# Optimization experiments

Measured on AMD Instinct MI355X. Metric: run time of the kernel, lower is better.

The kernel has to match this reference:

```python
import jax, jax.numpy as jnp
import numpy as np

HEAD_DIM = 16

def setup_inputs() -> dict:
    key = jax.random.key(0)
    ks = jax.random.split(key, 9)
    dim = 256
    B, H, W = 8, 32, 32
    x  = jax.random.normal(ks[0], (B, H, W, dim), jnp.float32)
    # Conv2d weights in OIHW layout (torch convention), small init
    w3 = jax.random.normal(ks[1], (dim, dim, 1, 1), jnp.float32) * 0.05
    b3 = jax.random.normal(ks[2], (dim,), jnp.float32) * 0.01
    w5 = jax.random.normal(ks[3], (dim, dim, 3, 3), jnp.float32) * 0.02
    b5 = jax.random.normal(ks[4], (dim,), jnp.float32) * 0.01
    w7 = jax.random.normal(ks[5], (dim, dim, 5, 5), jnp.float32) * 0.01
    b7 = jax.random.normal(ks[6], (dim,), jnp.float32) * 0.01
    # nn.Linear weight: (out_features=dim, in_features=attention_dim=dim), no bias
    wp = jax.random.normal(ks[7], (dim, dim), jnp.float32) * 0.05
    return {"x": x, "w3": w3, "b3": b3, "w5": w5, "b5": b5, "w7": w7, "b7": b7, "wp": wp}

def _conv2d_same(x_nchw, w_oihw, b):
    y = jax.lax.conv_general_dilated(
        x_nchw, w_oihw, window_strides=(1, 1), padding='SAME',
        dimension_numbers=('NCHW', 'OIHW', 'NCHW'))
    return y + b[None, :, None, None]

def reference(x, w3, b3, w5, b5, w7, b7, wp):
    B, H, W, C = x.shape
    N = H * W
    nh = C // HEAD_DIM            # num_heads
    scale = HEAD_DIM ** (-0.5)
    xc = jnp.transpose(x, (0, 3, 1, 2))  # NCHW
    # q: 1x1 conv, v: 3x3 conv, k: 5x5 conv (names match the torch code)
    q = _conv2d_same(xc, w3, b3).reshape(B, nh, N, HEAD_DIM)
    v = _conv2d_same(xc, w5, b5).reshape(B, nh, N, HEAD_DIM)
    k = _conv2d_same(xc, w7, b7).reshape(B, nh, N, HEAD_DIM)
    attn = jax.nn.softmax(jnp.einsum('bhnd,bhmd->bhnm', q, k) * scale, axis=-1)
    out = jnp.einsum('bhnm,bhmd->bhnd', attn, v)        # [B, nh, N, hd]
    out = jnp.transpose(out, (0, 2, 1, 3)).reshape(B, H, W, nh * HEAD_DIM)
    return out @ wp.T                                   # Linear, no bias
```

## Files before the change

kernel.cpp:

```cpp
#include <hip/hip_runtime.h>
#include <hip/hip_bf16.h>

#define DIM 256
#define HW  1024

typedef __attribute__((ext_vector_type(8))) short short8;
typedef __attribute__((ext_vector_type(4))) float floatx4;
typedef __attribute__((ext_vector_type(16))) float floatx16;
typedef __attribute__((address_space(1))) const unsigned int g_u32;
typedef __attribute__((address_space(3))) unsigned int l_u32;

#define QSCALE 0.36067376022224085f

__device__ inline unsigned short f2bf(float f) {
  union { float f; unsigned u; } v;
  v.f = f;
  unsigned u = v.u;
  u += 0x7fffu + ((u >> 16) & 1u);
  return (unsigned short)(u >> 16);
}

__device__ inline unsigned short f2bf_trunc(float f) {
  union { float f; unsigned u; } v;
  v.f = f;
  return (unsigned short)(v.u >> 16);
}

__device__ inline float ldin(const void* p, long i, int isf32) {
  if (isf32) return ((const float*)p)[i];
  union { unsigned u; float f; } v;
  v.u = ((unsigned)((const unsigned short*)p)[i]) << 16;
  return v.f;
}

__device__ inline int detect_inline(const unsigned short* __restrict__ xr,
                                    int* cnt) {
  if (threadIdx.x == 0) *cnt = 0;
  __syncthreads();
  int local = 0;
  for (int i = threadIdx.x; i < 8192; i += 256) {
    unsigned short u = xr[i];
    if ((u & 0x7F80u) == 0x7F80u) local++;
  }
  if (local) atomicAdd(cnt, local);
  __syncthreads();
  return (*cnt > 0) ? 1 : 0;
}

__device__ inline void frag_repack4(const void* __restrict__ w,
                                    unsigned short* __restrict__ wF, int KK,
                                    int slice, float* __restrict__ Wl,
                                    int isf32) {
  const int t = threadIdx.x;
  const int co16 = slice & 15;
  const int c8   = slice >> 4;
  const int RE = 32 * KK;
  const int RS = RE + 1;
  for (int g = 0; g < 4; ++g) {
    __syncthreads();
    for (int rloc = 0; rloc < 4; ++rloc) {
      const long base =
          ((long)((co16 * 16 + (g << 2) + rloc) * 256 + c8 * 32)) * KK;
      for (int i = t; i < RE; i += 256)
        Wl[rloc * RS + i] = ldin(w, base + i, isf32);
    }
    __syncthreads();
    for (int tap = 0; tap < KK; ++tap) {
      unsigned short* dst = wF + ((((tap << 3) + c8) << 4) + co16) * 512;
      if (t < 128) {
        const int colg = t >> 5;
        const int cis  = t & 31;
        const int col  = (g << 2) + colg;
        const int lane = ((cis >> 3) << 4) | col;
        const int j    = cis & 7;
        dst[lane * 8 + j] = f2bf(Wl[colg * RS + cis * KK + tap]);
      }
    }
  }
}

__global__ __launch_bounds__(256) void prep_kernel(
    const void* __restrict__ x,  const void* __restrict__ w3,
    const void* __restrict__ b3, const void* __restrict__ w5,
    const void* __restrict__ b5, const void* __restrict__ w7,
    const void* __restrict__ b7, const void* __restrict__ wp,
    unsigned short* __restrict__ xbf,
    unsigned short* __restrict__ wF3, unsigned short* __restrict__ wF5,
    unsigned short* __restrict__ wF7, unsigned short* __restrict__ wpF,
    float* __restrict__ bc, int* __restrict__ flag) {
  __shared__ float Wl[4 * 801];
  __shared__ int cnt;
  const int isf32 = detect_inline((const unsigned short*)x, &cnt);
  const int bid = blockIdx.x;
  const int t = threadIdx.x;
  if (bid < 512) {
#pragma unroll
    for (int r = 0; r < 4; ++r) {
      const int i = (bid * 1024 + r * 256 + t) * 4;
      if (isf32) {
        const float4 v = *(const float4*)((const float*)x + i);
        ushort4 o;
        o.x = f2bf(v.x); o.y = f2bf(v.y); o.z = f2bf(v.z); o.w = f2bf(v.w);
        *(ushort4*)(xbf + i) = o;
      } else {
        *(ushort4*)(xbf + i) =
            *(const ushort4*)((const unsigned short*)x + i);
      }
    }
  } else if (bid < 640) {
    frag_repack4(w7, wF7, 25, bid - 512, Wl, isf32);
  } else if (bid < 768) {
    frag_repack4(w5, wF5, 9, bid - 640, Wl, isf32);
  } else if (bid < 896) {
    frag_repack4(w3, wF3, 1, bid - 768, Wl, isf32);
  } else if (bid < 1024) {
    frag_repack4(wp, wpF, 1, bid - 896, Wl, isf32);
  } else {
#pragma unroll
    for (int r = 0; r < 3; ++r) {
      const int i = r * 256 + t;
      const void* src = (i < 256) ? b3 : (i < 512) ? b5 : b7;
      bc[i] = ldin(src, i & 255, isf32);
    }
    if (t == 0) *flag = isf32;
  }
}

__global__ __launch_bounds__(256, 2) void convqkv_kernel(
    const unsigned short* __restrict__ xbf,
    const unsigned short* __restrict__ wFq,
    const unsigned short* __restrict__ wFv,
    const unsigned short* __restrict__ wFk,
    const float* __restrict__ bc,
    unsigned short* __restrict__ qOut,
    unsigned short* __restrict__ vOut,
    unsigned short* __restrict__ kOut) {
  constexpr int WC = 36;
  constexpr int CELLS = 12 * WC;
  constexpr int LOADS = CELLS * 4;
  __shared__ unsigned short Xs[CELLS * 40];
  __shared__ unsigned short Bs[36 * 512];
  const int t    = threadIdx.x;
  const int bid  = blockIdx.x;
  const int cog0 = bid & 15;
  const int co0  = cog0 << 4;
  const int m0   = (bid >> 4) << 8;
  const int b    = m0 >> 10;
  const int n0   = m0 & 1023;
  const int r0   = n0 >> 5;
  const int wv   = t >> 6;
  const int lane = t & 63;
  const int l15  = lane & 15;
  const int quad = lane >> 4;

  floatx4 aq[4] = {}, av[4] = {}, ak[4] = {};

  for (int c8 = 0; c8 < 8; ++c8) {
    uint4 xreg[7];
#pragma unroll
    for (int rr = 0; rr < 7; ++rr) {
      const int id = rr * 256 + t;
      const int cell = id >> 2, part = id & 3;
      const int hr = cell / WC, wc = cell - hr * WC;
      const int xr = r0 + hr - 2, xc = wc - 2;
      const bool ok = (id < LOADS) && ((unsigned)xr < 32u) &&
                      ((unsigned)xc < 32u);
      const int cr = xr < 0 ? 0 : (xr > 31 ? 31 : xr);
      const int cc = xc < 0 ? 0 : (xc > 31 ? 31 : xc);
      uint4 v = *(const uint4*)&xbf[(((b * 32 + cr) * 32 + cc) << 8) +
                                    (c8 << 5) + (part << 3)];
      if (!ok) v = make_uint4(0, 0, 0, 0);
      xreg[rr] = v;
    }
    __syncthreads();
#pragma unroll
    for (int rr = 0; rr < 9; ++rr) {
      const int tap = (rr << 2) + wv;
      if (tap < 35) {
        const unsigned short* src;
        if (tap < 25) {
          src = &wFk[((((tap << 3) + c8) << 4) + cog0) * 512];
        } else if (tap < 34) {
          src = &wFv[(((((tap - 25) << 3) + c8) << 4) + cog0) * 512];
        } else {
          src = &wFq[((c8 << 4) + cog0) * 512];
        }
        __builtin_amdgcn_global_load_lds((g_u32*)(src + (lane << 3)),
                                         (l_u32*)&Bs[tap << 9], 16, 0, 0);
      }
    }
#pragma unroll
    for (int rr = 0; rr < 7; ++rr) {
      const int id = rr * 256 + t;
      if (id < LOADS)
        *(uint4*)&Xs[(id >> 2) * 40 + ((id & 3) << 3)] = xreg[rr];
    }
    __syncthreads();

#pragma unroll
    for (int tap = 0; tap < 25; ++tap) {
      const int kh = tap / 5, kw = tap % 5;
      const bool vv = (kh >= 1 && kh <= 3 && kw >= 1 && kw <= 3);
      short8 a[4];
#pragma unroll
      for (int rr2 = 0; rr2 < 2; ++rr2) {
#pragma unroll
        for (int ch = 0; ch < 2; ++ch) {
          const unsigned short* xs =
              &Xs[(((wv << 1) + rr2 + kh) * WC + (ch << 4) + l15 + kw) * 40 +
                  (quad << 3)];
          a[(rr2 << 1) + ch] = *(const short8*)xs;
        }
      }
      const short8 kb = *(const short8*)&Bs[(tap << 9) + (lane << 3)];
#pragma unroll
      for (int f = 0; f < 4; ++f)
        ak[f] = __builtin_amdgcn_mfma_f32_16x16x32_bf16(a[f], kb, ak[f],
                                                        0, 0, 0);
      if (vv) {
        const int vt = (kh - 1) * 3 + (kw - 1);
        const short8 vb = *(const short8*)&Bs[((25 + vt) << 9) + (lane << 3)];
#pragma unroll
        for (int f = 0; f < 4; ++f)
          av[f] = __builtin_amdgcn_mfma_f32_16x16x32_bf16(a[f], vb, av[f],
                                                          0, 0, 0);
      }
      if (tap == 12) {
        const short8 qb = *(const short8*)&Bs[(34 << 9) + (lane << 3)];
#pragma unroll
        for (int f = 0; f < 4; ++f)
          aq[f] = __builtin_amdgcn_mfma_f32_16x16x32_bf16(a[f], qb, aq[f],
                                                          0, 0, 0);
      }
    }
  }
#pragma unroll
  for (int rr2 = 0; rr2 < 2; ++rr2) {
#pragma unroll
    for (int ch = 0; ch < 2; ++ch) {
      const int f = (rr2 << 1) + ch;
      const int co = co0 + l15;
      const int slab = (b << 4) + (co >> 4);
      const int clo = co & 15;
      const int nb = n0 + (wv << 6) + (rr2 << 5) + (ch << 4) + (quad << 2);
      {
        const float bj = bc[co];
        floatx4 a = aq[f];
        ushort4 pk4;
        pk4.x = f2bf((a[0] + bj) * QSCALE);
        pk4.y = f2bf((a[1] + bj) * QSCALE);
        pk4.z = f2bf((a[2] + bj) * QSCALE);
        pk4.w = f2bf((a[3] + bj) * QSCALE);
        *(ushort4*)&qOut[(slab << 14) + (clo << 10) + nb] = pk4;
      }
      {
        const float bj = bc[512 + co];
        floatx4 a = ak[f];
        ushort4 pk4;
        pk4.x = f2bf(a[0] + bj); pk4.y = f2bf(a[1] + bj);
        pk4.z = f2bf(a[2] + bj); pk4.w = f2bf(a[3] + bj);
        *(ushort4*)&kOut[(slab << 14) + (clo << 10) + nb] = pk4;
      }
      {
        const float bj = bc[256 + co];
        floatx4 a = av[f];
        const int base = (slab << 14) + (clo << 6);
#pragma unroll
        for (int i = 0; i < 4; ++i) {
          const int n = nb + i;
          vOut[base + ((n & 15) << 10) + (n >> 4)] = f2bf(a[i] + bj);
        }
      }
    }
  }
}

__global__ __launch_bounds__(256, 4) void attn_mfma_kernel(
    const unsigned short* __restrict__ qg,
    const unsigned short* __restrict__ kg,
    const unsigned short* __restrict__ vg,
    unsigned short* __restrict__ out2) {
  __shared__ __align__(16) unsigned short Pb[4][32][40];
  const int t    = threadIdx.x;
  const int w    = t >> 6;
  const int lane = t & 63;
  const int slab = blockIdx.x >> 3;
  const int rb   = blockIdx.x & 7;
  const int b = slab >> 4;
  const int h = slab & 15;
  const int l31  = lane & 31;
  const int hl   = lane >> 5;
  const int l15  = lane & 15;
  const int quad = lane >> 4;

  const unsigned short* Kb = kg + (slab << 14);
  const unsigned short* Vb = vg + (slab << 14);

  const int row0 = (rb << 7) + (w << 5);
  const short8 qa =
      *(const short8*)&qg[(slab << 14) + ((row0 + l31) << 4) + (hl << 3)];

  const short onebf = (short)0x3F80;
  const short8 ones = {onebf, onebf, onebf, onebf, onebf, onebf, onebf, onebf};

  floatx4 acco[2] = {}, asum[2] = {};

  for (int kc = 0; kc < 1024; kc += 32) {
    const short8 kb = *(const short8*)&Kb[((kc + l31) << 4) + (hl << 3)];
    floatx16 s = {};
    s = __builtin_amdgcn_mfma_f32_32x32x16_bf16(qa, kb, s, 0, 0, 0);
#pragma unroll
    for (int r = 0; r < 16; ++r) {
      const float e = __builtin_amdgcn_exp2f(s[r]);
      const int row = (r & 3) + ((r >> 2) << 3) + (hl << 2);
      Pb[w][row][l31] = f2bf_trunc(e);
    }
    const short8 vb = *(const short8*)&Vb[(l15 << 10) + kc + (quad << 3)];
#pragma unroll
    for (int tt = 0; tt < 2; ++tt) {
      const short8 pa = *(const short8*)&Pb[w][(tt << 4) + l15][quad << 3];
      acco[tt] =
          __builtin_amdgcn_mfma_f32_16x16x32_bf16(pa, vb, acco[tt], 0, 0, 0);
      asum[tt] =
          __builtin_amdgcn_mfma_f32_16x16x32_bf16(pa, ones, asum[tt], 0, 0, 0);
    }
  }
#pragma unroll
  for (int tt = 0; tt < 2; ++tt) {
#pragma unroll
    for (int r = 0; r < 4; ++r) {
      const int nloc = (tt << 4) + (quad << 2) + r;
      const float val = acco[tt][r] / asum[tt][r];
      const int n = row0 + nloc;
      out2[(((b << 10) + n) << 8) + (h << 4) + l15] = f2bf(val);
    }
  }
}

__global__ __launch_bounds__(256) void linear_mfma_kernel(
    const unsigned short* __restrict__ inp,
    const unsigned short* __restrict__ wpF,
    void* __restrict__ out, const int* __restrict__ flag) {
  __shared__ unsigned short As[64 * 40];
  const int isf32 = *flag;
  const int t   = threadIdx.x;
  const int m0  = blockIdx.x << 6;
  const int co0 = blockIdx.y << 6;
  const int wv   = t >> 6;
  const int lane = t & 63;
  const int wm = (wv & 1) << 5;
  const int wn = (wv >> 1) << 5;
  const int l15  = lane & 15;
  const int quad = lane >> 4;
  const int cogb = (co0 >> 4) + (wn >> 4);
  const int rowS = t >> 2;
  const int partS = t & 3;

  floatx4 acc[2][2] = {};

  short8 cb0, cb1;
  {
    const unsigned short* wptr = &wpF[(cogb << 9) + (lane << 3)];
    cb0 = *(const short8*)wptr;
    cb1 = *(const short8*)(wptr + 512);
  }
  for (int c8 = 0; c8 < 8; ++c8) {
    const uint4 v = *(const uint4*)&inp[((m0 + rowS) << 8) + (c8 << 5) +
                                        (partS << 3)];
    short8 nb0 = {}, nb1 = {};
    if (c8 + 1 < 8) {
      const unsigned short* wptr =
          &wpF[((((c8 + 1) << 4) + cogb) << 9) + (lane << 3)];
      nb0 = *(const short8*)wptr;
      nb1 = *(const short8*)(wptr + 512);
    }
    __syncthreads();
    *(uint4*)&As[rowS * 40 + (partS << 3)] = v;
    __syncthreads();
    const unsigned short* xs = &As[(wm + l15) * 40 + (quad << 3)];
    const short8 afr0 = *(const short8*)xs;
    const short8 afr1 = *(const short8*)(xs + 16 * 40);
    acc[0][0] = __builtin_amdgcn_mfma_f32_16x16x32_bf16(afr0, cb0,
                                                        acc[0][0], 0, 0, 0);
    acc[0][1] = __builtin_amdgcn_mfma_f32_16x16x32_bf16(afr0, cb1,
                                                        acc[0][1], 0, 0, 0);
    acc[1][0] = __builtin_amdgcn_mfma_f32_16x16x32_bf16(afr1, cb0,
                                                        acc[1][0], 0, 0, 0);
    acc[1][1] = __builtin_amdgcn_mfma_f32_16x16x32_bf16(afr1, cb1,
                                                        acc[1][1], 0, 0, 0);
    cb0 = nb0; cb1 = nb1;
  }
#pragma unroll
  for (int mi = 0; mi < 2; ++mi) {
#pragma unroll
    for (int ni = 0; ni < 2; ++ni) {
      const int co = co0 + wn + (ni << 4) + l15;
      const int mb = m0 + wm + (mi << 4) + (quad << 2);
      floatx4 a = acc[mi][ni];
      if (!isf32) {
        unsigned short* o16 = (unsigned short*)out;
#pragma unroll
        for (int r = 0; r < 4; ++r) o16[(mb + r) * 256 + co] = f2bf(a[r]);
      } else {
        float* o32 = (float*)out;
#pragma unroll
        for (int r = 0; r < 4; ++r) o32[(mb + r) * 256 + co] = a[r];
      }
    }
  }
}

extern "C" void kernel_launch(void* const* d_in, const int* in_sizes, int n_in,
                              void* d_out, int out_size, void* d_ws,
                              size_t ws_size, hipStream_t stream) {
  const void* x  = d_in[0];
  const void* w3 = d_in[1];
  const void* b3 = d_in[2];
  const void* w5 = d_in[3];
  const void* b5 = d_in[4];
  const void* w7 = d_in[5];
  const void* b7 = d_in[6];
  const void* wp = d_in[7];

  char* p = (char*)d_ws;
  int* flag = (int*)p;                       p += 256;
  unsigned short* xbf = (unsigned short*)p;  p += 4u * 1024 * 1024;
  unsigned short* wF3 = (unsigned short*)p;  p += 131072;
  unsigned short* wF5 = (unsigned short*)p;  p += 1179648;
  unsigned short* wF7 = (unsigned short*)p;  p += 3276800;
  unsigned short* wpF = (unsigned short*)p;  p += 131072;
  float* bc = (float*)p;                     p += 4096;
  unsigned short* qc  = (unsigned short*)p;  p += 4194304;
  unsigned short* kT  = (unsigned short*)p;  p += 4194304;
  unsigned short* vT  = (unsigned short*)p;  p += 4194304;
  unsigned short* o2b = (unsigned short*)p;  p += 4194304;

  prep_kernel<<<1025, 256, 0, stream>>>(x, w3, b3, w5, b5, w7, b7, wp, xbf,
                                        wF3, wF5, wF7, wpF, bc, flag);

  convqkv_kernel<<<512, 256, 0, stream>>>(xbf, wF3, wF5, wF7, bc, qc, vT, kT);

  attn_mfma_kernel<<<1024, 256, 0, stream>>>(qc, kT, vT, o2b);

  dim3 lg(128, 4);
  linear_mfma_kernel<<<lg, 256, 0, stream>>>(o2b, wpF, d_out, flag);
}
```

Baseline: 174.6 us.

## Widen conv tile to two output-channel groups and load weights directly from global

```diff
diff --git a/kernel.cpp b/kernel.cpp
--- a/kernel.cpp
+++ b/kernel.cpp
@@ -126,7 +126,7 @@
   }
 }
 
-__global__ __launch_bounds__(256, 2) void convqkv_kernel(
+__global__ __launch_bounds__(256, 1) void convqkv_kernel(
     const unsigned short* __restrict__ xbf,
     const unsigned short* __restrict__ wFq,
     const unsigned short* __restrict__ wFv,
@@ -139,12 +139,12 @@
   constexpr int CELLS = 12 * WC;
   constexpr int LOADS = CELLS * 4;
   __shared__ unsigned short Xs[CELLS * 40];
-  __shared__ unsigned short Bs[36 * 512];
   const int t    = threadIdx.x;
   const int bid  = blockIdx.x;
-  const int cog0 = bid & 15;
-  const int co0  = cog0 << 4;
-  const int m0   = (bid >> 4) << 8;
+  const int cp   = bid & 7;
+  const int cog0 = cp << 1;
+  const int co0  = cp << 5;
+  const int m0   = (bid >> 3) << 8;
   const int b    = m0 >> 10;
   const int n0   = m0 & 1023;
   const int r0   = n0 >> 5;
@@ -153,7 +153,7 @@
   const int l15  = lane & 15;
   const int quad = lane >> 4;
 
-  floatx4 aq[4] = {}, av[4] = {}, ak[4] = {};
+  floatx4 aq[4][2] = {}, av[4][2] = {}, ak[4][2] = {};
 
   for (int c8 = 0; c8 < 8; ++c8) {
     uint4 xreg[7];
@@ -174,22 +174,6 @@
     }
     __syncthreads();
 #pragma unroll
-    for (int rr = 0; rr < 9; ++rr) {
-      const int tap = (rr << 2) + wv;
-      if (tap < 35) {
-        const unsigned short* src;
-        if (tap < 25) {
-          src = &wFk[((((tap << 3) + c8) << 4) + cog0) * 512];
-        } else if (tap < 34) {
-          src = &wFv[(((((tap - 25) << 3) + c8) << 4) + cog0) * 512];
-        } else {
-          src = &wFq[((c8 << 4) + cog0) * 512];
-        }
-        __builtin_amdgcn_global_load_lds((g_u32*)(src + (lane << 3)),
-                                         (l_u32*)&Bs[tap << 9], 16, 0, 0);
-      }
-    }
-#pragma unroll
     for (int rr = 0; rr < 7; ++rr) {
       const int id = rr * 256 + t;
       if (id < LOADS)
@@ -212,25 +196,43 @@
           a[(rr2 << 1) + ch] = *(const short8*)xs;
         }
       }
-      const short8 kb = *(const short8*)&Bs[(tap << 9) + (lane << 3)];
-#pragma unroll
-      for (int f = 0; f < 4; ++f)
-        ak[f] = __builtin_amdgcn_mfma_f32_16x16x32_bf16(a[f], kb, ak[f],
-                                                        0, 0, 0);
+      const unsigned short* bk =
+          &wFk[(((((tap << 3) + c8) << 4) + cog0) << 9) + (lane << 3)];
+      const short8 kb0 = *(const short8*)bk;
+      const short8 kb1 = *(const short8*)(bk + 512);
+#pragma unroll
+      for (int f = 0; f < 4; ++f) {
+        ak[f][0] = __builtin_amdgcn_mfma_f32_16x16x32_bf16(a[f], kb0,
+                                                           ak[f][0], 0, 0, 0);
+        ak[f][1] = __builtin_amdgcn_mfma_f32_16x16x32_bf16(a[f], kb1,
+                                                           ak[f][1], 0, 0, 0);
+      }
       if (vv) {
         const int vt = (kh - 1) * 3 + (kw - 1);
-        const short8 vb = *(const short8*)&Bs[((25 + vt) << 9) + (lane << 3)];
-#pragma unroll
-        for (int f = 0; f < 4; ++f)
-          av[f] = __builtin_amdgcn_mfma_f32_16x16x32_bf16(a[f], vb, av[f],
-                                                          0, 0, 0);
+        const unsigned short* bv =
+            &wFv[(((((vt << 3) + c8) << 4) + cog0) << 9) + (lane << 3)];
+        const short8 vb0 = *(const short8*)bv;
+        const short8 vb1 = *(const short8*)(bv + 512);
+#pragma unroll
+        for (int f = 0; f < 4; ++f) {
+          av[f][0] = __builtin_amdgcn_mfma_f32_16x16x32_bf16(a[f], vb0,
+                                                             av[f][0], 0, 0, 0);
+          av[f][1] = __builtin_amdgcn_mfma_f32_16x16x32_bf16(a[f], vb1,
+                                                             av[f][1], 0, 0, 0);
+        }
       }
       if (tap == 12) {
-        const short8 qb = *(const short8*)&Bs[(34 << 9) + (lane << 3)];
-#pragma unroll
-        for (int f = 0; f < 4; ++f)
-          aq[f] = __builtin_amdgcn_mfma_f32_16x16x32_bf16(a[f], qb, aq[f],
-                                                          0, 0, 0);
+        const unsigned short* bq =
+            &wFq[(((c8 << 4) + cog0) << 9) + (lane << 3)];
+        const short8 qb0 = *(const short8*)bq;
+        const short8 qb1 = *(const short8*)(bq + 512);
+#pragma unroll
+        for (int f = 0; f < 4; ++f) {
+          aq[f][0] = __builtin_amdgcn_mfma_f32_16x16x32_bf16(a[f], qb0,
+                                                             aq[f][0], 0, 0, 0);
+          aq[f][1] = __builtin_amdgcn_mfma_f32_16x16x32_bf16(a[f], qb1,
+                                                             aq[f][1], 0, 0, 0);
+        }
       }
     }
   }
@@ -239,36 +241,39 @@
 #pragma unroll
     for (int ch = 0; ch < 2; ++ch) {
       const int f = (rr2 << 1) + ch;
-      const int co = co0 + l15;
-      const int slab = (b << 4) + (co >> 4);
-      const int clo = co & 15;
       const int nb = n0 + (wv << 6) + (rr2 << 5) + (ch << 4) + (quad << 2);
-      {
-        const float bj = bc[co];
-        floatx4 a = aq[f];
-        ushort4 pk4;
-        pk4.x = f2bf((a[0] + bj) * QSCALE);
-        pk4.y = f2bf((a[1] + bj) * QSCALE);
-        pk4.z = f2bf((a[2] + bj) * QSCALE);
-        pk4.w = f2bf((a[3] + bj) * QSCALE);
-        *(ushort4*)&qOut[(slab << 14) + (clo << 10) + nb] = pk4;
-      }
-      {
-        const float bj = bc[512 + co];
-        floatx4 a = ak[f];
-        ushort4 pk4;
-        pk4.x = f2bf(a[0] + bj); pk4.y = f2bf(a[1] + bj);
-        pk4.z = f2bf(a[2] + bj); pk4.w = f2bf(a[3] + bj);
-        *(ushort4*)&kOut[(slab << 14) + (clo << 10) + nb] = pk4;
-      }
-      {
-        const float bj = bc[256 + co];
-        floatx4 a = av[f];
-        const int base = (slab << 14) + (clo << 6);
-#pragma unroll
-        for (int i = 0; i < 4; ++i) {
-          const int n = nb + i;
-          vOut[base + ((n & 15) << 10) + (n >> 4)] = f2bf(a[i] + bj);
+#pragma unroll
+      for (int ni = 0; ni < 2; ++ni) {
+        const int co = co0 + (ni << 4) + l15;
+        const int slab = (b << 4) + (co >> 4);
+        const int clo = co & 15;
+        {
+          const float bj = bc[co];
+          floatx4 a = aq[f][ni];
+          ushort4 pk4;
+          pk4.x = f2bf((a[0] + bj) * QSCALE);
+          pk4.y = f2bf((a[1] + bj) * QSCALE);
+          pk4.z = f2bf((a[2] + bj) * QSCALE);
+          pk4.w = f2bf((a[3] + bj) * QSCALE);
+          *(ushort4*)&qOut[(slab << 14) + (clo << 10) + nb] = pk4;
+        }
+        {
+          const float bj = bc[512 + co];
+          floatx4 a = ak[f][ni];
+          ushort4 pk4;
+          pk4.x = f2bf(a[0] + bj); pk4.y = f2bf(a[1] + bj);
+          pk4.z = f2bf(a[2] + bj); pk4.w = f2bf(a[3] + bj);
+          *(ushort4*)&kOut[(slab << 14) + (clo << 10) + nb] = pk4;
+        }
+        {
+          const float bj = bc[256 + co];
+          floatx4 a = av[f][ni];
+          const int base = (slab << 14) + (clo << 6);
+#pragma unroll
+          for (int i = 0; i < 4; ++i) {
+            const int n = nb + i;
+            vOut[base + ((n & 15) << 10) + (n >> 4)] = f2bf(a[i] + bj);
+          }
         }
       }
     }
@@ -438,7 +443,7 @@
   prep_kernel<<<1025, 256, 0, stream>>>(x, w3, b3, w5, b5, w7, b7, wp, xbf,
                                         wF3, wF5, wF7, wpF, bc, flag);
 
-  convqkv_kernel<<<512, 256, 0, stream>>>(xbf, wF3, wF5, wF7, bc, qc, vT, kT);
+  convqkv_kernel<<<256, 256, 0, stream>>>(xbf, wF3, wF5, wF7, bc, qc, vT, kT);
 
   attn_mfma_kernel<<<1024, 256, 0, stream>>>(qc, kT, vT, o2b);
 
```

Measured after the change: 240.5 us. 1.38x slower.

## Reuse conv input fragments across kernel rows and pack softmax probabilities with cvt_pk

Applied to the files above, without the earlier changes.

```diff
diff --git a/kernel.cpp b/kernel.cpp
--- a/kernel.cpp
+++ b/kernel.cpp
@@ -198,39 +198,57 @@
     __syncthreads();
 
 #pragma unroll
-    for (int tap = 0; tap < 25; ++tap) {
-      const int kh = tap / 5, kw = tap % 5;
-      const bool vv = (kh >= 1 && kh <= 3 && kw >= 1 && kw <= 3);
-      short8 a[4];
-#pragma unroll
-      for (int rr2 = 0; rr2 < 2; ++rr2) {
+    for (int kw = 0; kw < 5; ++kw) {
+      short8 a[6][2];
+#pragma unroll
+      for (int ri = 0; ri < 6; ++ri) {
 #pragma unroll
         for (int ch = 0; ch < 2; ++ch) {
           const unsigned short* xs =
-              &Xs[(((wv << 1) + rr2 + kh) * WC + (ch << 4) + l15 + kw) * 40 +
+              &Xs[(((wv << 1) + ri) * WC + (ch << 4) + l15 + kw) * 40 +
                   (quad << 3)];
-          a[(rr2 << 1) + ch] = *(const short8*)xs;
-        }
-      }
-      const short8 kb = *(const short8*)&Bs[(tap << 9) + (lane << 3)];
-#pragma unroll
-      for (int f = 0; f < 4; ++f)
-        ak[f] = __builtin_amdgcn_mfma_f32_16x16x32_bf16(a[f], kb, ak[f],
-                                                        0, 0, 0);
-      if (vv) {
-        const int vt = (kh - 1) * 3 + (kw - 1);
-        const short8 vb = *(const short8*)&Bs[((25 + vt) << 9) + (lane << 3)];
-#pragma unroll
-        for (int f = 0; f < 4; ++f)
-          av[f] = __builtin_amdgcn_mfma_f32_16x16x32_bf16(a[f], vb, av[f],
-                                                          0, 0, 0);
-      }
-      if (tap == 12) {
-        const short8 qb = *(const short8*)&Bs[(34 << 9) + (lane << 3)];
-#pragma unroll
-        for (int f = 0; f < 4; ++f)
-          aq[f] = __builtin_amdgcn_mfma_f32_16x16x32_bf16(a[f], qb, aq[f],
-                                                          0, 0, 0);
+          a[ri][ch] = *(const short8*)xs;
+        }
+      }
+#pragma unroll
+      for (int kh = 0; kh < 5; ++kh) {
+        const int tap = kh * 5 + kw;
+        const short8 kb = *(const short8*)&Bs[(tap << 9) + (lane << 3)];
+#pragma unroll
+        for (int rr2 = 0; rr2 < 2; ++rr2) {
+#pragma unroll
+          for (int ch = 0; ch < 2; ++ch) {
+            const int f = (rr2 << 1) + ch;
+            ak[f] = __builtin_amdgcn_mfma_f32_16x16x32_bf16(
+                a[rr2 + kh][ch], kb, ak[f], 0, 0, 0);
+          }
+        }
+        if (kh >= 1 && kh <= 3 && kw >= 1 && kw <= 3) {
+          const int vt = (kh - 1) * 3 + (kw - 1);
+          const short8 vb =
+              *(const short8*)&Bs[((25 + vt) << 9) + (lane << 3)];
+#pragma unroll
+          for (int rr2 = 0; rr2 < 2; ++rr2) {
+#pragma unroll
+            for (int ch = 0; ch < 2; ++ch) {
+              const int f = (rr2 << 1) + ch;
+              av[f] = __builtin_amdgcn_mfma_f32_16x16x32_bf16(
+                  a[rr2 + kh][ch], vb, av[f], 0, 0, 0);
+            }
+          }
+        }
+        if (tap == 12) {
+          const short8 qb = *(const short8*)&Bs[(34 << 9) + (lane << 3)];
+#pragma unroll
+          for (int rr2 = 0; rr2 < 2; ++rr2) {
+#pragma unroll
+            for (int ch = 0; ch < 2; ++ch) {
+              const int f = (rr2 << 1) + ch;
+              aq[f] = __builtin_amdgcn_mfma_f32_16x16x32_bf16(
+                  a[rr2 + kh][ch], qb, aq[f], 0, 0, 0);
+            }
+          }
+        }
       }
     }
   }
@@ -308,12 +326,18 @@
   for (int kc = 0; kc < 1024; kc += 32) {
     const short8 kb = *(const short8*)&Kb[((kc + l31) << 4) + (hl << 3)];
     floatx16 s = {};
-    s = __builtin_amdgcn_mfma_f32_32x32x16_bf16(qa, kb, s, 0, 0, 0);
-#pragma unroll
-    for (int r = 0; r < 16; ++r) {
-      const float e = __builtin_amdgcn_exp2f(s[r]);
-      const int row = (r & 3) + ((r >> 2) << 3) + (hl << 2);
-      Pb[w][row][l31] = f2bf_trunc(e);
+    s = __builtin_amdgcn_mfma_f32_32x32x16_bf16(kb, qa, s, 0, 0, 0);
+#pragma unroll
+    for (int g = 0; g < 4; ++g) {
+      const float e0 = __builtin_amdgcn_exp2f(s[(g << 2) + 0]);
+      const float e1 = __builtin_amdgcn_exp2f(s[(g << 2) + 1]);
+      const float e2 = __builtin_amdgcn_exp2f(s[(g << 2) + 2]);
+      const float e3 = __builtin_amdgcn_exp2f(s[(g << 2) + 3]);
+      unsigned lo, hi;
+      asm("v_cvt_pk_bf16_f32 %0, %1, %2" : "=v"(lo) : "v"(e0), "v"(e1));
+      asm("v_cvt_pk_bf16_f32 %0, %1, %2" : "=v"(hi) : "v"(e2), "v"(e3));
+      uint2 pk; pk.x = lo; pk.y = hi;
+      *(uint2*)&Pb[w][l31][(g << 3) + (hl << 2)] = pk;
     }
     const short8 vb = *(const short8*)&Vb[(l15 << 10) + kc + (quad << 3)];
 #pragma unroll
```

After: 170.8 us (median of 2 runs). 2.2% less time.

## Transpose QK MFMA to pack P stores, remap conv X staging, add setprio

Applied to the files above, without the earlier changes.

```diff
diff --git a/kernel.cpp b/kernel.cpp
--- a/kernel.cpp
+++ b/kernel.cpp
@@ -137,7 +137,6 @@
     unsigned short* __restrict__ kOut) {
   constexpr int WC = 36;
   constexpr int CELLS = 12 * WC;
-  constexpr int LOADS = CELLS * 4;
   __shared__ unsigned short Xs[CELLS * 40];
   __shared__ unsigned short Bs[36 * 512];
   const int t    = threadIdx.x;
@@ -160,10 +159,12 @@
 #pragma unroll
     for (int rr = 0; rr < 7; ++rr) {
       const int id = rr * 256 + t;
-      const int cell = id >> 2, part = id & 3;
+      const int grp = id >> 6;
+      const int part = grp & 3;
+      const int cell = ((grp >> 2) << 6) + (id & 63);
       const int hr = cell / WC, wc = cell - hr * WC;
       const int xr = r0 + hr - 2, xc = wc - 2;
-      const bool ok = (id < LOADS) && ((unsigned)xr < 32u) &&
+      const bool ok = (cell < CELLS) && ((unsigned)xr < 32u) &&
                       ((unsigned)xc < 32u);
       const int cr = xr < 0 ? 0 : (xr > 31 ? 31 : xr);
       const int cc = xc < 0 ? 0 : (xc > 31 ? 31 : xc);
@@ -192,8 +193,10 @@
 #pragma unroll
     for (int rr = 0; rr < 7; ++rr) {
       const int id = rr * 256 + t;
-      if (id < LOADS)
-        *(uint4*)&Xs[(id >> 2) * 40 + ((id & 3) << 3)] = xreg[rr];
+      const int grp = id >> 6;
+      const int cell = ((grp >> 2) << 6) + (id & 63);
+      if (cell < CELLS)
+        *(uint4*)&Xs[cell * 40 + ((grp & 3) << 3)] = xreg[rr];
     }
     __syncthreads();
 
@@ -308,14 +311,23 @@
   for (int kc = 0; kc < 1024; kc += 32) {
     const short8 kb = *(const short8*)&Kb[((kc + l31) << 4) + (hl << 3)];
     floatx16 s = {};
-    s = __builtin_amdgcn_mfma_f32_32x32x16_bf16(qa, kb, s, 0, 0, 0);
-#pragma unroll
-    for (int r = 0; r < 16; ++r) {
-      const float e = __builtin_amdgcn_exp2f(s[r]);
-      const int row = (r & 3) + ((r >> 2) << 3) + (hl << 2);
-      Pb[w][row][l31] = f2bf_trunc(e);
+    __builtin_amdgcn_s_setprio(1);
+    s = __builtin_amdgcn_mfma_f32_32x32x16_bf16(kb, qa, s, 0, 0, 0);
+    __builtin_amdgcn_s_setprio(0);
+#pragma unroll
+    for (int g = 0; g < 4; ++g) {
+      const float e0 = __builtin_amdgcn_exp2f(s[(g << 2) + 0]);
+      const float e1 = __builtin_amdgcn_exp2f(s[(g << 2) + 1]);
+      const float e2 = __builtin_amdgcn_exp2f(s[(g << 2) + 2]);
+      const float e3 = __builtin_amdgcn_exp2f(s[(g << 2) + 3]);
+      unsigned lo, hi;
+      asm("v_cvt_pk_bf16_f32 %0, %1, %2" : "=v"(lo) : "v"(e0), "v"(e1));
+      asm("v_cvt_pk_bf16_f32 %0, %1, %2" : "=v"(hi) : "v"(e2), "v"(e3));
+      uint2 pk; pk.x = lo; pk.y = hi;
+      *(uint2*)&Pb[w][l31][(g << 3) + (hl << 2)] = pk;
     }
     const short8 vb = *(const short8*)&Vb[(l15 << 10) + kc + (quad << 3)];
+    __builtin_amdgcn_s_setprio(1);
 #pragma unroll
     for (int tt = 0; tt < 2; ++tt) {
       const short8 pa = *(const short8*)&Pb[w][(tt << 4) + l15][quad << 3];
@@ -324,6 +336,7 @@
       asum[tt] =
           __builtin_amdgcn_mfma_f32_16x16x32_bf16(pa, ones, asum[tt], 0, 0, 0);
     }
+    __builtin_amdgcn_s_setprio(0);
   }
 #pragma unroll
   for (int tt = 0; tt < 2; ++tt) {
```

After: 176.6 us. Within noise of the previous version (+1.1%).
